# Kernel tuning notes

Measured on AMD Instinct MI355X. Metric: run time of the kernel, lower is better.

## Reference

```python
import jax, jax.numpy as jnp
import numpy as np

K = 31  # box-filter kernel size
PAD = 15

def _avg_pool_31(x):
    # count_include_pad=True (torch default): divide by K*K everywhere
    s = jax.lax.reduce_window(x, 0.0, jax.lax.add,
                              window_dimensions=(1, 1, K, K),
                              window_strides=(1, 1, 1, 1),
                              padding=((0, 0), (0, 0), (PAD, PAD), (PAD, PAD)))
    return s / (K * K)

def setup_inputs() -> dict:
    key = jax.random.key(0)
    k1, k2 = jax.random.split(key)
    pred = jax.random.normal(k1, (64, 1, 512, 512), dtype=jnp.float32)
    mask = jax.random.uniform(k2, (64, 1, 512, 512), dtype=jnp.float32)
    return {"pred": pred, "mask": mask}

def reference(pred, mask):
    weight = 1.0 + 5.0 * jnp.abs(_avg_pool_31(mask) - mask)
    # binary_cross_entropy_with_logits, reduction='none' (stable form)
    bce = jnp.maximum(pred, 0.0) - pred * mask + jnp.log1p(jnp.exp(-jnp.abs(pred)))
    p = jax.nn.sigmoid(pred)
    inter = p * mask
    union = p + mask
    iou = 1.0 - (inter + 1.0) / (union - inter + 1.0)
    wsum = weight.sum(axis=(2, 3))  # [B, C]
    weighted_bce = (weight * bce).sum(axis=(2, 3)) / wsum
    weighted_iou = (weight * iou).sum(axis=(2, 3)) / wsum
    return (weighted_bce + weighted_iou).mean()
```

## Files before the change

kernel.cpp:

```cpp
#include <hip/hip_runtime.h>
#include <math.h>

#define BATCH 64
#define H 512
#define W 512
#define KRAD 15
#define STRIP 64
#define NSTRIP (H / STRIP)
#define RING 64

__device__ __forceinline__ float wave_reduce(float v) {
    #pragma unroll
    for (int off = 32; off > 0; off >>= 1) v += __shfl_xor(v, off);
    return v;
}

__device__ __forceinline__ unsigned bf16b(float f) {
    unsigned u = __float_as_uint(f);
    return (u + 0x7FFFu + ((u >> 16) & 1u)) >> 16;
}
__device__ __forceinline__ float fbf16(unsigned short s) {
    return __uint_as_float(((unsigned)s) << 16);
}

__device__ __forceinline__ void scan_row(const float* __restrict__ img_base, int r,
                                         int lane, unsigned short* dst) {
    float o[8];
    if (0 <= r && r < H) {
        const float4* in4 = reinterpret_cast<const float4*>(img_base + (size_t)r * W + lane * 8);
        float4 va = in4[0], vb = in4[1];
        float v[8] = {va.x, va.y, va.z, va.w, vb.x, vb.y, vb.z, vb.w};
        float P[8];
        float run = 0.f;
        #pragma unroll
        for (int k = 0; k < 8; ++k) { run += v[k]; P[k] = run; }
        float scan = run;
        #pragma unroll
        for (int off = 1; off < 64; off <<= 1) {
            float n = __shfl_up(scan, off);
            if (lane >= off) scan += n;
        }
        const float excl = scan - run;
        #pragma unroll
        for (int k = 0; k < 8; ++k) P[k] += excl;
        const float total = __shfl(P[7], 63);
        float shA[8], shB[8];
        shA[0] = __shfl_down(P[7], 1);
        #pragma unroll
        for (int k = 1; k < 8; ++k) shA[k] = __shfl_down(P[k - 1], 2);
        #pragma unroll
        for (int k = 0; k < 8; ++k) shB[k] = __shfl_up(P[k], 2);
        const int xb = lane * 8;
        #pragma unroll
        for (int k = 0; k < 8; ++k) {
            const int x = xb + k;
            const float A  = (x + KRAD <= W - 1) ? shA[k] : total;
            const float Bv = (x >= KRAD + 1) ? shB[k] : 0.f;
            o[k] = A - Bv;
        }
    } else {
        #pragma unroll
        for (int k = 0; k < 8; ++k) o[k] = 0.f;
    }
    uint4 wv;
    wv.x = bf16b(o[0]) | (bf16b(o[1]) << 16);
    wv.y = bf16b(o[2]) | (bf16b(o[3]) << 16);
    wv.z = bf16b(o[4]) | (bf16b(o[5]) << 16);
    wv.w = bf16b(o[6]) | (bf16b(o[7]) << 16);
    *reinterpret_cast<uint4*>(dst + lane * 8) = wv;
}

__global__ __launch_bounds__(512) void fused_kernel(const float* __restrict__ pred,
                                                    const float* __restrict__ mask,
                                                    float2* __restrict__ partials) {
    __shared__ unsigned short ring[RING][W];
    __shared__ float2 wacc[8];

    const int tid  = threadIdx.x;
    const int wave = tid >> 6;
    const int lane = tid & 63;
    const int img   = blockIdx.x >> 3;
    const int strip = blockIdx.x & 7;
    const int r0 = strip * STRIP;
    const int c  = tid;
    const float* mk = mask + (size_t)img * H * W;
    const float* pr = pred + (size_t)img * H * W;

    #pragma unroll
    for (int gp = 0; gp < 4; ++gp) {
        const int idx = gp * 8 + wave;
        if (idx < 31) {
            const int r = r0 - 16 + idx;
            scan_row(mk, r, lane, &ring[r & (RING - 1)][0]);
        }
    }
    __syncthreads();

    float vsum = 0.f;
    #pragma unroll
    for (int j = 0; j < 30; ++j) {
        vsum += fbf16(ring[(r0 - 15 + j) & (RING - 1)][c]);
    }

    float s0 = 0.f, s1 = 0.f;
    const float inv_k2 = 1.0f / 961.0f;

    for (int g = 0; g < STRIP / 8; ++g) {
        const int ybase = r0 + g * 8;
        {
            const int r = ybase + 15 + wave;
            scan_row(mk, r, lane, &ring[r & (RING - 1)][0]);
        }
        __syncthreads();

        float addv[8], subv[8], m[8], p[8];
        #pragma unroll
        for (int i = 0; i < 8; ++i) {
            addv[i] = fbf16(ring[(ybase + i + 15) & (RING - 1)][c]);
            subv[i] = fbf16(ring[(ybase + i - 16) & (RING - 1)][c]);
        }
        #pragma unroll
        for (int i = 0; i < 8; ++i) {
            m[i] = mk[(size_t)(ybase + i) * W + c];
            p[i] = pr[(size_t)(ybase + i) * W + c];
        }
        #pragma unroll
        for (int i = 0; i < 8; ++i) {
            vsum += addv[i] - subv[i];
            const float avg = vsum * inv_k2;
            const float w = 1.0f + 5.0f * fabsf(avg - m[i]);
            const float e = __expf(-fabsf(p[i]));
            const float softplus = __logf(1.0f + e);
            const float bce = fmaxf(p[i], 0.0f) - p[i] * m[i] + softplus;
            const float r1pe = __builtin_amdgcn_rcpf(1.0f + e);
            const float sig = (p[i] >= 0.0f) ? r1pe : e * r1pe;
            const float inter = sig * m[i];
            const float denom = sig + m[i] - inter + 1.0f;
            const float iou = 1.0f - (inter + 1.0f) * __builtin_amdgcn_rcpf(denom);
            s0 += w;
            s1 += w * (bce + iou);
        }
        __syncthreads();
    }

    s0 = wave_reduce(s0);
    s1 = wave_reduce(s1);
    if (lane == 0) wacc[wave] = make_float2(s0, s1);
    __syncthreads();
    if (tid == 0) {
        float a0 = 0.f, a1 = 0.f;
        #pragma unroll
        for (int i = 0; i < 8; ++i) { a0 += wacc[i].x; a1 += wacc[i].y; }
        partials[blockIdx.x] = make_float2(a0, a1);
    }
}

__global__ void finalize_kernel(const float2* __restrict__ partials,
                                float* __restrict__ out) {
    const int lane = threadIdx.x;
    float s0 = 0.f, s1 = 0.f;
    #pragma unroll
    for (int j = 0; j < NSTRIP; ++j) {
        const float2 pp = partials[lane * NSTRIP + j];
        s0 += pp.x; s1 += pp.y;
    }
    float q = s1 / s0;
    q = wave_reduce(q);
    if (lane == 0) out[0] = q * (1.0f / (float)BATCH);
}

extern "C" void kernel_launch(void* const* d_in, const int* in_sizes, int n_in,
                              void* d_out, int out_size, void* d_ws, size_t ws_size,
                              hipStream_t stream) {
    const float* pred = (const float*)d_in[0];
    const float* mask = (const float*)d_in[1];
    float2* partials = (float2*)d_ws;

    hipLaunchKernelGGL(fused_kernel, dim3(BATCH * NSTRIP), dim3(512), 0, stream,
                       pred, mask, partials);
    hipLaunchKernelGGL(finalize_kernel, dim3(1), dim3(64), 0, stream,
                       partials, (float*)d_out);
}
```

Baseline: 44.99 us.

## Halve strip height, shrink LDS ring, and software-pipeline mask row loads

Cuts the strip from 64 to 32 rows and the ring buffer from 64 to 40 rows, which doubles the block count and lowers LDS per block to 40 KB so more blocks can share a CU (launch bounds now request 8). Mask row loads are split from the prefix-scan so the next row's global load is issued before the current row is scanned, overlapping memory latency with compute. It also fully unrolls the strip loop with constant ring slot indices, replaces __syncthreads with a lighter lgkmcnt wait plus s_barrier, and reuses the ring memory for the wave partials. In exchange each strip's 31-row halo is recomputed twice as often, adding redundant scan work and extra mask reads.

After: 115.0 us. 156% more time.

```diff
diff --git a/kernel.cpp b/kernel.cpp
--- a/kernel.cpp
+++ b/kernel.cpp
@@ -5,14 +5,20 @@
 #define H 512
 #define W 512
 #define KRAD 15
-#define STRIP 64
+#define STRIP 32
 #define NSTRIP (H / STRIP)
-#define RING 64
+#define RING 40
 
 __device__ __forceinline__ float wave_reduce(float v) {
     #pragma unroll
     for (int off = 32; off > 0; off >>= 1) v += __shfl_xor(v, off);
     return v;
+}
+
+__device__ __forceinline__ void lds_barrier() {
+    asm volatile("s_waitcnt lgkmcnt(0)" ::: "memory");
+    __builtin_amdgcn_s_barrier();
+    asm volatile("" ::: "memory");
 }
 
 __device__ __forceinline__ unsigned bf16b(float f) {
@@ -23,106 +29,122 @@
     return __uint_as_float(((unsigned)s) << 16);
 }
 
-__device__ __forceinline__ void scan_row(const float* __restrict__ img_base, int r,
-                                         int lane, unsigned short* dst) {
+__device__ __forceinline__ void load_row(const float* __restrict__ base, int r, int lane,
+                                         float4& a, float4& b) {
+    if (0 <= r && r < H) {
+        const float4* p4 = reinterpret_cast<const float4*>(base + (size_t)r * W + lane * 8);
+        a = p4[0]; b = p4[1];
+    } else {
+        a = make_float4(0.f, 0.f, 0.f, 0.f);
+        b = a;
+    }
+}
+
+__device__ __forceinline__ void scan_store(float4 va, float4 vb, int lane,
+                                           unsigned short* dst) {
+    float v[8] = {va.x, va.y, va.z, va.w, vb.x, vb.y, vb.z, vb.w};
+    float P[8];
+    float run = 0.f;
+    #pragma unroll
+    for (int k = 0; k < 8; ++k) { run += v[k]; P[k] = run; }
+    float scan = run;
+    #pragma unroll
+    for (int off = 1; off < 64; off <<= 1) {
+        float n = __shfl_up(scan, off);
+        if (lane >= off) scan += n;
+    }
+    const float excl = scan - run;
+    #pragma unroll
+    for (int k = 0; k < 8; ++k) P[k] += excl;
+    const float total = __shfl(P[7], 63);
+    float shA[8], shB[8];
+    shA[0] = __shfl_down(P[7], 1);
+    #pragma unroll
+    for (int k = 1; k < 8; ++k) shA[k] = __shfl_down(P[k - 1], 2);
+    #pragma unroll
+    for (int k = 0; k < 8; ++k) shB[k] = __shfl_up(P[k], 2);
+    const int xb = lane * 8;
     float o[8];
-    if (0 <= r && r < H) {
-        const float4* in4 = reinterpret_cast<const float4*>(img_base + (size_t)r * W + lane * 8);
-        float4 va = in4[0], vb = in4[1];
-        float v[8] = {va.x, va.y, va.z, va.w, vb.x, vb.y, vb.z, vb.w};
-        float P[8];
-        float run = 0.f;
-        #pragma unroll
-        for (int k = 0; k < 8; ++k) { run += v[k]; P[k] = run; }
-        float scan = run;
-        #pragma unroll
-        for (int off = 1; off < 64; off <<= 1) {
-            float n = __shfl_up(scan, off);
-            if (lane >= off) scan += n;
-        }
-        const float excl = scan - run;
-        #pragma unroll
-        for (int k = 0; k < 8; ++k) P[k] += excl;
-        const float total = __shfl(P[7], 63);
-        float shA[8], shB[8];
-        shA[0] = __shfl_down(P[7], 1);
-        #pragma unroll
-        for (int k = 1; k < 8; ++k) shA[k] = __shfl_down(P[k - 1], 2);
-        #pragma unroll
-        for (int k = 0; k < 8; ++k) shB[k] = __shfl_up(P[k], 2);
-        const int xb = lane * 8;
-        #pragma unroll
-        for (int k = 0; k < 8; ++k) {
-            const int x = xb + k;
-            const float A  = (x + KRAD <= W - 1) ? shA[k] : total;
-            const float Bv = (x >= KRAD + 1) ? shB[k] : 0.f;
-            o[k] = A - Bv;
-        }
-    } else {
-        #pragma unroll
-        for (int k = 0; k < 8; ++k) o[k] = 0.f;
+    #pragma unroll
+    for (int k = 0; k < 8; ++k) {
+        const int x = xb + k;
+        const float A  = (x + KRAD <= W - 1) ? shA[k] : total;
+        const float Bv = (x >= KRAD + 1) ? shB[k] : 0.f;
+        o[k] = A - Bv;
     }
     uint4 wv;
     wv.x = bf16b(o[0]) | (bf16b(o[1]) << 16);
     wv.y = bf16b(o[2]) | (bf16b(o[3]) << 16);
     wv.z = bf16b(o[4]) | (bf16b(o[5]) << 16);
     wv.w = bf16b(o[6]) | (bf16b(o[7]) << 16);
-    *reinterpret_cast<uint4*>(dst + lane * 8) = wv;
-}
-
-__global__ __launch_bounds__(512) void fused_kernel(const float* __restrict__ pred,
-                                                    const float* __restrict__ mask,
-                                                    float2* __restrict__ partials) {
+    *reinterpret_cast<uint4*>(dst + xb) = wv;
+}
+
+__global__ __launch_bounds__(512, 8) void fused_kernel(const float* __restrict__ pred,
+                                                       const float* __restrict__ mask,
+                                                       float2* __restrict__ partials) {
     __shared__ unsigned short ring[RING][W];
-    __shared__ float2 wacc[8];
 
     const int tid  = threadIdx.x;
     const int wave = tid >> 6;
     const int lane = tid & 63;
-    const int img   = blockIdx.x >> 3;
-    const int strip = blockIdx.x & 7;
+    const int img   = blockIdx.x >> 4;
+    const int strip = blockIdx.x & 15;
     const int r0 = strip * STRIP;
     const int c  = tid;
-    const float* mk = mask + (size_t)img * H * W;
-    const float* pr = pred + (size_t)img * H * W;
-
-    #pragma unroll
-    for (int gp = 0; gp < 4; ++gp) {
-        const int idx = gp * 8 + wave;
-        if (idx < 31) {
-            const int r = r0 - 16 + idx;
-            scan_row(mk, r, lane, &ring[r & (RING - 1)][0]);
-        }
-    }
-    __syncthreads();
+    const float* mk = mask + (size_t)img * (H * W);
+    const float* pr = pred + (size_t)img * (H * W);
+
+    {
+        float4 pa, pb;
+        int pidx = wave;
+        load_row(mk, r0 - 16 + pidx, lane, pa, pb);
+        #pragma unroll
+        for (int gp = 0; gp < 4; ++gp) {
+            float4 na, nb;
+            const int nidx = pidx + 8;
+            if (gp < 3 && nidx < 31) load_row(mk, r0 - 16 + nidx, lane, na, nb);
+            if (pidx < 31) scan_store(pa, pb, lane, &ring[pidx][0]);
+            pa = na; pb = nb; pidx = nidx;
+        }
+    }
+
+    float4 sva, svb;
+    load_row(mk, r0 + 15 + wave, lane, sva, svb);
+
+    lds_barrier();
 
     float vsum = 0.f;
     #pragma unroll
-    for (int j = 0; j < 30; ++j) {
-        vsum += fbf16(ring[(r0 - 15 + j) & (RING - 1)][c]);
-    }
+    for (int s = 1; s <= 30; ++s) vsum += fbf16(ring[s][c]);
 
     float s0 = 0.f, s1 = 0.f;
     const float inv_k2 = 1.0f / 961.0f;
 
+    #pragma unroll
     for (int g = 0; g < STRIP / 8; ++g) {
-        const int ybase = r0 + g * 8;
         {
-            const int r = ybase + 15 + wave;
-            scan_row(mk, r, lane, &ring[r & (RING - 1)][0]);
-        }
-        __syncthreads();
+            const int off = 8 * g + 31 + wave;
+            const int slot = (off >= RING) ? off - RING : off;
+            scan_store(sva, svb, lane, &ring[slot][0]);
+        }
+        if (g + 1 < STRIP / 8) load_row(mk, r0 + 8 * (g + 1) + 15 + wave, lane, sva, svb);
+
+        lds_barrier();
 
         float addv[8], subv[8], m[8], p[8];
         #pragma unroll
         for (int i = 0; i < 8; ++i) {
-            addv[i] = fbf16(ring[(ybase + i + 15) & (RING - 1)][c]);
-            subv[i] = fbf16(ring[(ybase + i - 16) & (RING - 1)][c]);
+            const int offA = 8 * g + 31 + i;
+            const int slotA = (offA >= RING) ? offA - RING : offA;
+            addv[i] = fbf16(ring[slotA][c]);
+            subv[i] = fbf16(ring[8 * g + i][c]);
         }
         #pragma unroll
         for (int i = 0; i < 8; ++i) {
-            m[i] = mk[(size_t)(ybase + i) * W + c];
-            p[i] = pr[(size_t)(ybase + i) * W + c];
+            const int y = r0 + 8 * g + i;
+            m[i] = mk[(size_t)y * W + c];
+            p[i] = pr[(size_t)y * W + c];
         }
         #pragma unroll
         for (int i = 0; i < 8; ++i) {
@@ -140,11 +162,12 @@
             s0 += w;
             s1 += w * (bce + iou);
         }
-        __syncthreads();
+        lds_barrier();
     }
 
     s0 = wave_reduce(s0);
     s1 = wave_reduce(s1);
+    float2* wacc = reinterpret_cast<float2*>(&ring[0][0]);
     if (lane == 0) wacc[wave] = make_float2(s0, s1);
     __syncthreads();
     if (tid == 0) {
```

## Halve strip height and shrink ring buffer to raise block count and occupancy

Applied to the files above, without the earlier changes.

Halves the rows each block processes, from 64 to 32, which doubles the grid to 1024 blocks, and shrinks the LDS ring from 64 to 40 rows so more blocks fit per CU. Ring slots now come from compile-time offsets relative to the strip start instead of masked absolute row indices, and the main loop is fully unrolled. The per-wave accumulator array now reuses the ring's LDS instead of a separate buffer. The cost is more redundant halo row scans (31 rows per 32 output rows instead of per 64), which means extra mask reads and prefix-scan work.

After: 64.59 us. 1.44x slower.

```diff
diff --git a/kernel.cpp b/kernel.cpp
--- a/kernel.cpp
+++ b/kernel.cpp
@@ -5,9 +5,9 @@
 #define H 512
 #define W 512
 #define KRAD 15
-#define STRIP 64
+#define STRIP 32
 #define NSTRIP (H / STRIP)
-#define RING 64
+#define RING 40
 
 __device__ __forceinline__ float wave_reduce(float v) {
     #pragma unroll
@@ -74,55 +74,53 @@
                                                     const float* __restrict__ mask,
                                                     float2* __restrict__ partials) {
     __shared__ unsigned short ring[RING][W];
-    __shared__ float2 wacc[8];
 
     const int tid  = threadIdx.x;
     const int wave = tid >> 6;
     const int lane = tid & 63;
-    const int img   = blockIdx.x >> 3;
-    const int strip = blockIdx.x & 7;
+    const int img   = blockIdx.x >> 4;
+    const int strip = blockIdx.x & 15;
     const int r0 = strip * STRIP;
     const int c  = tid;
-    const float* mk = mask + (size_t)img * H * W;
-    const float* pr = pred + (size_t)img * H * W;
+    const float* mk = mask + (size_t)img * (H * W);
+    const float* pr = pred + (size_t)img * (H * W);
 
     #pragma unroll
     for (int gp = 0; gp < 4; ++gp) {
         const int idx = gp * 8 + wave;
-        if (idx < 31) {
-            const int r = r0 - 16 + idx;
-            scan_row(mk, r, lane, &ring[r & (RING - 1)][0]);
-        }
+        if (idx < 31) scan_row(mk, r0 - 16 + idx, lane, &ring[idx][0]);
     }
     __syncthreads();
 
     float vsum = 0.f;
     #pragma unroll
-    for (int j = 0; j < 30; ++j) {
-        vsum += fbf16(ring[(r0 - 15 + j) & (RING - 1)][c]);
-    }
+    for (int s = 1; s <= 30; ++s) vsum += fbf16(ring[s][c]);
 
     float s0 = 0.f, s1 = 0.f;
     const float inv_k2 = 1.0f / 961.0f;
 
+    #pragma unroll
     for (int g = 0; g < STRIP / 8; ++g) {
-        const int ybase = r0 + g * 8;
         {
-            const int r = ybase + 15 + wave;
-            scan_row(mk, r, lane, &ring[r & (RING - 1)][0]);
+            const int off = 8 * g + 31 + wave;
+            const int slot = (off >= RING) ? off - RING : off;
+            scan_row(mk, r0 + 8 * g + 15 + wave, lane, &ring[slot][0]);
         }
         __syncthreads();
 
         float addv[8], subv[8], m[8], p[8];
         #pragma unroll
         for (int i = 0; i < 8; ++i) {
-            addv[i] = fbf16(ring[(ybase + i + 15) & (RING - 1)][c]);
-            subv[i] = fbf16(ring[(ybase + i - 16) & (RING - 1)][c]);
+            const int offA = 8 * g + 31 + i;
+            const int slotA = (offA >= RING) ? offA - RING : offA;
+            addv[i] = fbf16(ring[slotA][c]);
+            subv[i] = fbf16(ring[8 * g + i][c]);
         }
         #pragma unroll
         for (int i = 0; i < 8; ++i) {
-            m[i] = mk[(size_t)(ybase + i) * W + c];
-            p[i] = pr[(size_t)(ybase + i) * W + c];
+            const int y = r0 + 8 * g + i;
+            m[i] = mk[(size_t)y * W + c];
+            p[i] = pr[(size_t)y * W + c];
         }
         #pragma unroll
         for (int i = 0; i < 8; ++i) {
@@ -145,6 +143,7 @@
 
     s0 = wave_reduce(s0);
     s1 = wave_reduce(s1);
+    float2* wacc = reinterpret_cast<float2*>(&ring[0][0]);
     if (lane == 0) wacc[wave] = make_float2(s0, s1);
     __syncthreads();
     if (tid == 0) {
```
